# Kernel optimization log

Hardware: AMD Instinct MI355X
Metric: run time of the kernel (lower is better)

## Reference

```python
import jax, jax.numpy as jnp
import numpy as np

NUM_HEADS = 12
HEAD_SIZE = 64
N_EMBED = 768
SEQ_LEN = 2048
BATCH = 4


def setup_inputs() -> dict:
    key = jax.random.key(0)
    ks = jax.random.split(key, 7)
    s = 0.02
    x = jax.random.normal(ks[0], (BATCH, SEQ_LEN, N_EMBED), dtype=jnp.float32)
    # per-head bias-free q/k/v projections: [H, E, D]
    Wq = jax.random.normal(ks[1], (NUM_HEADS, N_EMBED, HEAD_SIZE), dtype=jnp.float32) * s
    Wk = jax.random.normal(ks[2], (NUM_HEADS, N_EMBED, HEAD_SIZE), dtype=jnp.float32) * s
    Wv = jax.random.normal(ks[3], (NUM_HEADS, N_EMBED, HEAD_SIZE), dtype=jnp.float32) * s
    # output projection: Linear(num_heads*head_size, n_embed)
    Wp = jax.random.normal(ks[4], (NUM_HEADS * HEAD_SIZE, N_EMBED), dtype=jnp.float32) * s
    bp = jax.random.normal(ks[5], (N_EMBED,), dtype=jnp.float32) * s
    return {"x": x, "Wq": Wq, "Wk": Wk, "Wv": Wv, "Wp": Wp, "bp": bp}


def reference(x, Wq, Wk, Wv, Wp, bp):
    B, S, E = x.shape
    scale = HEAD_SIZE ** -0.5
    # project all heads at once: [B,H,S,D]
    q = jnp.einsum("bse,hed->bhsd", x, Wq)
    k = jnp.einsum("bse,hed->bhsd", x, Wk)
    v = jnp.einsum("bse,hed->bhsd", x, Wv)
    # scaled dot-product scores [B,H,S,S] with causal mask
    scores = jnp.einsum("bhsd,bhtd->bhst", q, k) * scale
    causal = jnp.tril(jnp.ones((S, S), dtype=bool))
    scores = jnp.where(causal[None, None, :, :], scores, jnp.finfo(scores.dtype).min)
    attn = jax.nn.softmax(scores, axis=-1)
    out = jnp.einsum("bhst,bhtd->bhsd", attn, v)
    # concat heads along feature dim: [B,S,H*D]
    out = out.transpose(0, 2, 1, 3).reshape(B, S, NUM_HEADS * HEAD_SIZE)
    # final projection (dropout rate = 0.0)
    return out @ Wp + bp
```

## Files before the change

kernel.cpp:

```cpp
#include <hip/hip_runtime.h>
#include <hip/hip_bf16.h>


typedef __attribute__((ext_vector_type(8))) short bf16x8;
typedef __attribute__((ext_vector_type(4))) float f32x4;
typedef __attribute__((ext_vector_type(16))) float f32x16;
typedef __attribute__((ext_vector_type(4))) uint u32x4;

#define OFF_XB   0
#define OFF_WT   6291456
#define OFF_WPT  8060928
#define OFF_QKV  8650752
#define OFF_AO   27525120

#define SCALE_LOG2E 0.1803368801111204f

__device__ inline ushort f2bf(float f) {
  __hip_bfloat16 h = __float2bfloat16(f);
  return *reinterpret_cast<ushort*>(&h);
}
__device__ inline uint cvt_pk(float lo, float hi) {
  uint r;
  asm("v_cvt_pk_bf16_f32 %0, %1, %2" : "=v"(r) : "v"(lo), "v"(hi));
  return r;
}
#define GLOAD16(g, l)                                                              \
  __builtin_amdgcn_global_load_lds(                                                \
      (const __attribute__((address_space(1))) uint*)(g),                          \
      (__attribute__((address_space(3))) uint*)(l), 16, 0, 0)

#define WAITBAR(n) asm volatile("s_waitcnt vmcnt(" #n ")\ns_barrier" ::: "memory")
#define ENDBAR()   asm volatile("s_waitcnt lgkmcnt(0)\ns_barrier" ::: "memory")

__global__ __launch_bounds__(256) void cvt_bf16(const float* __restrict__ src,
                                                ushort* __restrict__ dst, int n8) {
  int i = blockIdx.x * 256 + threadIdx.x;
  if (i >= n8) return;
  float4 a = *(const float4*)&src[(size_t)i * 8];
  float4 b = *(const float4*)&src[(size_t)i * 8 + 4];
  u32x4 pk = {cvt_pk(a.x, a.y), cvt_pk(a.z, a.w), cvt_pk(b.x, b.y), cvt_pk(b.z, b.w)};
  *(bf16x8*)&dst[(size_t)i * 8] = __builtin_bit_cast(bf16x8, pk);
}

__global__ __launch_bounds__(256) void transpose_wqkv(const float* __restrict__ Wq,
                                                      const float* __restrict__ Wk,
                                                      const float* __restrict__ Wv,
                                                      ushort* __restrict__ dst) {
  __shared__ ushort tile[64][130];
  int mat = blockIdx.y;
  int te = blockIdx.x;
  const float* src = (mat < 12) ? Wq : (mat < 24) ? Wk : Wv;
  int m12 = mat % 12;
  size_t base = (size_t)m12 * 768 * 64;
  int t = threadIdx.x;
#pragma unroll
  for (int i = 0; i < 16; i++) {
    int idx = i * 256 + t;
    int r = idx >> 6, c = idx & 63;
    tile[r][c] = f2bf(src[base + (size_t)(te * 64 + r) * 64 + c]);
  }
  __syncthreads();
  size_t obase = (size_t)mat * 49152;
#pragma unroll
  for (int i = 0; i < 16; i++) {
    int idx = i * 256 + t;
    int c = idx >> 6, r = idx & 63;
    dst[obase + (size_t)c * 768 + te * 64 + r] = tile[r][c];
  }
}

__global__ __launch_bounds__(256) void transpose_w(const float* __restrict__ src,
                                                   ushort* __restrict__ dst,
                                                   int Edim, int Ddim) {
  __shared__ ushort tile[64][130];
  int ntd = Ddim >> 6;
  int te = blockIdx.x / ntd, td = blockIdx.x % ntd;
  int t = threadIdx.x;
#pragma unroll
  for (int i = 0; i < 16; i++) {
    int idx = i * 256 + t;
    int r = idx >> 6, c = idx & 63;
    tile[r][c] = f2bf(src[(size_t)(te * 64 + r) * Ddim + td * 64 + c]);
  }
  __syncthreads();
#pragma unroll
  for (int i = 0; i < 16; i++) {
    int idx = i * 256 + t;
    int c = idx >> 6, r = idx & 63;
    dst[(size_t)(td * 64 + c) * Edim + te * 64 + r] = tile[r][c];
  }
}

__device__ inline uint swz(uint row) { return (row + (row >> 2)) & 3; }

__global__ __launch_bounds__(128, 2) void gemm_qkv(const ushort* __restrict__ X,
                                                   const ushort* __restrict__ Wt,
                                                   ushort* __restrict__ qkv,
                                                   uint* __restrict__ vtg) {
  __shared__ ushort Ash[2][128 * 32];
  __shared__ ushort Bsh[2][128 * 32];
  int mb = blockIdx.x, nb = blockIdx.y;
  int t = threadIdx.x, w = t >> 6, lane = t & 63, lo = lane & 15, g = lane >> 4;
  const ushort* Ab = X + (size_t)mb * 128 * 768;
  const ushort* Bb = Wt + (size_t)nb * 128 * 768;
  f32x4 acc[4][8];
#pragma unroll
  for (int fi = 0; fi < 4; fi++)
#pragma unroll
    for (int fj = 0; fj < 8; fj++) acc[fi][fj] = (f32x4){0.f, 0.f, 0.f, 0.f};
  uint srow[4], ssc[4];
#pragma unroll
  for (int j = 0; j < 4; j++) {
    uint ci = j * 128 + t;
    srow[j] = ci >> 2;
    ssc[j] = ((ci & 3) ^ swz(ci >> 2)) << 4;
  }

#define QKV_STAGE(tile, bsel)                                                         \
  {                                                                                   \
    int e0 = (tile) * 32;                                                             \
    _Pragma("unroll")                                                                 \
    for (int j = 0; j < 4; j++) {                                                     \
      GLOAD16((const char*)(Ab + (size_t)srow[j] * 768 + e0) + ssc[j],                \
              &Ash[bsel][(j * 128 + w * 64) * 8]);                                    \
      GLOAD16((const char*)(Bb + (size_t)srow[j] * 768 + e0) + ssc[j],                \
              &Bsh[bsel][(j * 128 + w * 64) * 8]);                                    \
    }                                                                                 \
  }

  QKV_STAGE(0, 0);
  QKV_STAGE(1, 1);
  uint rsw = swz(lo) << 4;
  for (int it = 0; it < 24; ++it) {
    if (it < 23) { WAITBAR(8); } else { WAITBAR(0); }
    const ushort* Acur = Ash[it & 1];
    const ushort* Bcur = Bsh[it & 1];
    bf16x8 af[4], bf[8];
#pragma unroll
    for (int fi = 0; fi < 4; fi++) {
      int arow = w * 64 + fi * 16 + lo;
      af[fi] = *(const bf16x8*)((const char*)Acur + arow * 64 + ((g << 4) ^ rsw));
    }
#pragma unroll
    for (int fj = 0; fj < 8; fj++) {
      int brow = fj * 16 + lo;
      bf[fj] = *(const bf16x8*)((const char*)Bcur + brow * 64 + ((g << 4) ^ rsw));
    }
#pragma unroll
    for (int fi = 0; fi < 4; fi++)
#pragma unroll
      for (int fj = 0; fj < 8; fj++)
        acc[fi][fj] = __builtin_amdgcn_mfma_f32_16x16x32_bf16(af[fi], bf[fj], acc[fi][fj], 0, 0, 0);
    if (it < 22) {
      ENDBAR();
      QKV_STAGE(it + 2, it & 1);
    }
  }
#undef QKV_STAGE
#pragma unroll
  for (int fj = 0; fj < 8; fj++) {
    int mat = nb * 2 + (fj >> 2);
    int ty = mat / 12, h = mat % 12;
    int d = (fj & 3) * 16 + lo;
    if (ty < 2) {
#pragma unroll
      for (int fi = 0; fi < 4; fi++)
#pragma unroll
        for (int rr = 0; rr < 4; rr++) {
          int m = mb * 128 + w * 64 + fi * 16 + g * 4 + rr;
          int b = m >> 11, s = m & 2047;
          qkv[(size_t)ty * 6291456 + (size_t)(b * 12 + h) * 131072 + (size_t)s * 64 + d] =
              f2bf(acc[fi][fj][rr]);
        }
    } else {
#pragma unroll
      for (int fi = 0; fi < 4; fi++)
#pragma unroll
        for (int rr = 0; rr < 4; rr += 2) {
          int m = mb * 128 + w * 64 + fi * 16 + g * 4 + rr;
          int b = m >> 11, s = m & 2047;
          uint pk = cvt_pk(acc[fi][fj][rr], acc[fi][fj][rr + 1]);
          vtg[(size_t)(b * 12 + h) * 65536 + (s >> 6) * 2048 + d * 32 + ((s & 63) >> 1)] = pk;
        }
    }
  }
}

__global__ __launch_bounds__(256, 3) void attn_fwd(const ushort* __restrict__ Qg,
                                                   const ushort* __restrict__ Kg,
                                                   const uint* __restrict__ Vtg,
                                                   ushort* __restrict__ ao) {
  __shared__ ushort Ksh[2][64 * 72];
  __shared__ uint Vsh[2][64 * 36];
  int x = blockIdx.x;
  int head = x % 48;
  int qb = 15 - x / 48;
  int T = 2 * qb + 2;
  int t = threadIdx.x, w = t >> 6, q31 = t & 31, hi = (t & 63) >> 5;
  const ushort* Q = Qg + (size_t)head * 131072;
  const ushort* K = Kg + (size_t)head * 131072;
  const uint* V = Vtg + (size_t)head * 65536;
  int qstart = qb * 128 + 32 * w;
  int qg = qstart + q31;
  bf16x8 qf[4];
#pragma unroll
  for (int s = 0; s < 4; s++)
    qf[s] = *(const bf16x8*)&Q[(size_t)qg * 64 + s * 16 + hi * 8];
  bf16x8 ones;
#pragma unroll
  for (int i = 0; i < 8; i++) ones[i] = (short)0x3F80;
  f32x16 oacc[2], lacc;
#pragma unroll
  for (int r = 0; r < 16; r++) { oacc[0][r] = 0.f; oacc[1][r] = 0.f; lacc[r] = 0.f; }
  int sr = t >> 3, sc = t & 7;
  bf16x8 kreg[2];
  u32x4 vreg[2];
#pragma unroll
  for (int i = 0; i < 2; i++) {
    kreg[i] = *(const bf16x8*)&K[(size_t)(i * 32 + sr) * 64 + sc * 8];
    vreg[i] = *(const u32x4*)&V[(i * 32 + sr) * 32 + sc * 4];
  }
#pragma unroll
  for (int i = 0; i < 2; i++) {
    *(bf16x8*)&Ksh[0][(i * 32 + sr) * 72 + sc * 8] = kreg[i];
    *(u32x4*)&Vsh[0][(i * 32 + sr) * 36 + sc * 4] = vreg[i];
  }
  for (int kb = 0; kb < T; kb++) {
    __syncthreads();
    if (kb + 1 < T) {
      int t1 = (kb + 1) * 64;
#pragma unroll
      for (int i = 0; i < 2; i++) {
        kreg[i] = *(const bf16x8*)&K[(size_t)(t1 + i * 32 + sr) * 64 + sc * 8];
        vreg[i] = *(const u32x4*)&V[(kb + 1) * 2048 + (i * 32 + sr) * 32 + sc * 4];
      }
    }
    int t0 = kb * 64;
    if (t0 <= qstart + 31) {
      const ushort* Kb = Ksh[kb & 1];
      const uint* Vb = Vsh[kb & 1];
      bool act1 = (t0 + 32 <= qstart + 31);
      f32x16 st0, st1;
#pragma unroll
      for (int r = 0; r < 16; r++) { st0[r] = 0.f; st1[r] = 0.f; }
#pragma unroll
      for (int s = 0; s < 4; s++) {
        bf16x8 kf = *(const bf16x8*)&Kb[q31 * 72 + s * 16 + hi * 8];
        st0 = __builtin_amdgcn_mfma_f32_32x32x16_bf16(kf, qf[s], st0, 0, 0, 0);
      }
      if (act1) {
#pragma unroll
        for (int s = 0; s < 4; s++) {
          bf16x8 kf = *(const bf16x8*)&Kb[(32 + q31) * 72 + s * 16 + hi * 8];
          st1 = __builtin_amdgcn_mfma_f32_32x32x16_bf16(kf, qf[s], st1, 0, 0, 0);
        }
      }
      if (t0 + 31 > qstart) {
        int base = t0 - qstart;
#pragma unroll
        for (int r = 0; r < 16; r++) {
          int crow = (r & 3) + 8 * (r >> 2) + 4 * hi;
          if (base + crow > q31) st0[r] = -3e38f;
        }
      }
      if (act1 && (t0 + 63 > qstart)) {
        int base = t0 + 32 - qstart;
#pragma unroll
        for (int r = 0; r < 16; r++) {
          int crow = (r & 3) + 8 * (r >> 2) + 4 * hi;
          if (base + crow > q31) st1[r] = -3e38f;
        }
      }
#pragma unroll
      for (int r = 0; r < 16; r++)
        st0[r] = __builtin_amdgcn_exp2f(st0[r] * SCALE_LOG2E);
      if (act1) {
#pragma unroll
        for (int r = 0; r < 16; r++)
          st1[r] = __builtin_amdgcn_exp2f(st1[r] * SCALE_LOG2E);
      }
      int ns = act1 ? 4 : 2;
      bf16x8 paf[4];
#pragma unroll
      for (int s = 0; s < 4; s++) {
        if (s < ns) {
          const f32x16& sv = (s < 2) ? st0 : st1;
          int rb = (s & 1) * 8;
          uint a = cvt_pk(sv[rb + 0], sv[rb + 1]);
          uint b2 = cvt_pk(sv[rb + 2], sv[rb + 3]);
          uint c = cvt_pk(sv[rb + 4], sv[rb + 5]);
          uint d = cvt_pk(sv[rb + 6], sv[rb + 7]);
          asm volatile("v_permlane32_swap_b32 %0, %1" : "+v"(a), "+v"(c));
          asm volatile("v_permlane32_swap_b32 %0, %1" : "+v"(b2), "+v"(d));
          u32x4 u4 = {a, b2, c, d};
          paf[s] = __builtin_bit_cast(bf16x8, u4);
        }
      }
#pragma unroll
      for (int s = 0; s < 4; s++) {
        if (s < ns) {
          lacc = __builtin_amdgcn_mfma_f32_32x32x16_bf16(paf[s], ones, lacc, 0, 0, 0);
#pragma unroll
          for (int dt = 0; dt < 2; dt++) {
            bf16x8 vf = *(const bf16x8*)&Vb[(dt * 32 + q31) * 36 + s * 8 + hi * 4];
            oacc[dt] = __builtin_amdgcn_mfma_f32_32x32x16_bf16(paf[s], vf, oacc[dt], 0, 0, 0);
          }
        }
      }
    }
    if (kb + 1 < T) {
      int b2 = (kb + 1) & 1;
#pragma unroll
      for (int i = 0; i < 2; i++) {
        *(bf16x8*)&Ksh[b2][(i * 32 + sr) * 72 + sc * 8] = kreg[i];
        *(u32x4*)&Vsh[b2][(i * 32 + sr) * 36 + sc * 4] = vreg[i];
      }
    }
  }
  int hh = head % 12, bb = head / 12;
#pragma unroll
  for (int dt = 0; dt < 2; dt++)
#pragma unroll
    for (int r = 0; r < 16; r++) {
      int qr = qstart + (r & 3) + 8 * (r >> 2) + 4 * hi;
      ao[(size_t)(bb * 2048 + qr) * 768 + hh * 64 + dt * 32 + q31] =
          f2bf(oacc[dt][r] / lacc[r]);
    }
}

__global__ __launch_bounds__(128, 2) void gemm_out(const ushort* __restrict__ A,
                                                   const ushort* __restrict__ Bt,
                                                   const float* __restrict__ bias,
                                                   float* __restrict__ out) {
  __shared__ ushort Ash[2][128 * 32];
  __shared__ ushort Bsh[2][128 * 32];
  int mb = blockIdx.x, nb = blockIdx.y;
  int t = threadIdx.x, w = t >> 6, lane = t & 63, lo = lane & 15, g = lane >> 4;
  const ushort* Ab = A + (size_t)mb * 128 * 768;
  const ushort* Bb = Bt + (size_t)nb * 128 * 768;
  f32x4 acc[4][8];
#pragma unroll
  for (int fi = 0; fi < 4; fi++)
#pragma unroll
    for (int fj = 0; fj < 8; fj++) acc[fi][fj] = (f32x4){0.f, 0.f, 0.f, 0.f};
  uint srow[4], ssc[4];
#pragma unroll
  for (int j = 0; j < 4; j++) {
    uint ci = j * 128 + t;
    srow[j] = ci >> 2;
    ssc[j] = ((ci & 3) ^ swz(ci >> 2)) << 4;
  }

#define OUT_STAGE(tile, bsel)                                                         \
  {                                                                                   \
    int e0 = (tile) * 32;                                                             \
    _Pragma("unroll")                                                                 \
    for (int j = 0; j < 4; j++) {                                                     \
      GLOAD16((const char*)(Ab + (size_t)srow[j] * 768 + e0) + ssc[j],                \
              &Ash[bsel][(j * 128 + w * 64) * 8]);                                    \
      GLOAD16((const char*)(Bb + (size_t)srow[j] * 768 + e0) + ssc[j],                \
              &Bsh[bsel][(j * 128 + w * 64) * 8]);                                    \
    }                                                                                 \
  }

  OUT_STAGE(0, 0);
  OUT_STAGE(1, 1);
  uint rsw = swz(lo) << 4;
  for (int it = 0; it < 24; ++it) {
    if (it < 23) { WAITBAR(8); } else { WAITBAR(0); }
    const ushort* Acur = Ash[it & 1];
    const ushort* Bcur = Bsh[it & 1];
    bf16x8 af[4], bf[8];
#pragma unroll
    for (int fi = 0; fi < 4; fi++) {
      int arow = w * 64 + fi * 16 + lo;
      af[fi] = *(const bf16x8*)((const char*)Acur + arow * 64 + ((g << 4) ^ rsw));
    }
#pragma unroll
    for (int fj = 0; fj < 8; fj++) {
      int brow = fj * 16 + lo;
      bf[fj] = *(const bf16x8*)((const char*)Bcur + brow * 64 + ((g << 4) ^ rsw));
    }
#pragma unroll
    for (int fi = 0; fi < 4; fi++)
#pragma unroll
      for (int fj = 0; fj < 8; fj++)
        acc[fi][fj] = __builtin_amdgcn_mfma_f32_16x16x32_bf16(af[fi], bf[fj], acc[fi][fj], 0, 0, 0);
    if (it < 22) {
      ENDBAR();
      OUT_STAGE(it + 2, it & 1);
    }
  }
#undef OUT_STAGE
#pragma unroll
  for (int fj = 0; fj < 8; fj++) {
    int col = nb * 128 + fj * 16 + lo;
    float bv = bias[col];
#pragma unroll
    for (int fi = 0; fi < 4; fi++)
#pragma unroll
      for (int rr = 0; rr < 4; rr++) {
        int m = mb * 128 + w * 64 + fi * 16 + g * 4 + rr;
        out[(size_t)m * 768 + col] = acc[fi][fj][rr] + bv;
      }
  }
}

extern "C" void kernel_launch(void* const* d_in, const int* in_sizes, int n_in,
                              void* d_out, int out_size, void* d_ws, size_t ws_size,
                              hipStream_t stream) {
  const float* x  = (const float*)d_in[0];
  const float* Wq = (const float*)d_in[1];
  const float* Wk = (const float*)d_in[2];
  const float* Wv = (const float*)d_in[3];
  const float* Wp = (const float*)d_in[4];
  const float* bp = (const float*)d_in[5];
  float* out = (float*)d_out;
  ushort* ws = (ushort*)d_ws;

  ushort* xb  = ws + OFF_XB;
  ushort* wt  = ws + OFF_WT;
  ushort* wpt = ws + OFF_WPT;
  ushort* qkv = ws + OFF_QKV;
  uint*   vt  = (uint*)(ws + OFF_QKV + 2 * 6291456);
  ushort* ao  = ws + OFF_AO;

  cvt_bf16<<<dim3(3072), 256, 0, stream>>>(x, xb, 786432);
  transpose_wqkv<<<dim3(12, 36), 256, 0, stream>>>(Wq, Wk, Wv, wt);
  transpose_w<<<dim3(144), 256, 0, stream>>>(Wp, wpt, 768, 768);

  gemm_qkv<<<dim3(64, 18), 128, 0, stream>>>(xb, wt, qkv, vt);
  attn_fwd<<<dim3(768), 256, 0, stream>>>(qkv, qkv + 6291456, vt, ao);
  gemm_out<<<dim3(64, 6), 128, 0, stream>>>(ao, wpt, bp, out);
}
```

Measured before the change: 129.4 us.

## Give each wave private LDS tiles in projection GEMMs to drop barriers

After: 143.5 us. +10.9%, slower.

```diff
diff --git a/kernel.cpp b/kernel.cpp
--- a/kernel.cpp
+++ b/kernel.cpp
@@ -29,8 +29,8 @@
       (const __attribute__((address_space(1))) uint*)(g),                          \
       (__attribute__((address_space(3))) uint*)(l), 16, 0, 0)
 
-#define WAITBAR(n) asm volatile("s_waitcnt vmcnt(" #n ")\ns_barrier" ::: "memory")
-#define ENDBAR()   asm volatile("s_waitcnt lgkmcnt(0)\ns_barrier" ::: "memory")
+#define WAITN(n)  asm volatile("s_waitcnt vmcnt(" #n ")" ::: "memory")
+#define LGKM0()   asm volatile("s_waitcnt lgkmcnt(0)" ::: "memory")
 
 __global__ __launch_bounds__(256) void cvt_bf16(const float* __restrict__ src,
                                                 ushort* __restrict__ dst, int n8) {
@@ -93,58 +93,63 @@
 
 __device__ inline uint swz(uint row) { return (row + (row >> 2)) & 3; }
 
-__global__ __launch_bounds__(128, 2) void gemm_qkv(const ushort* __restrict__ X,
-                                                   const ushort* __restrict__ Wt,
-                                                   ushort* __restrict__ qkv,
-                                                   uint* __restrict__ vtg) {
-  __shared__ ushort Ash[2][128 * 32];
-  __shared__ ushort Bsh[2][128 * 32];
+__global__ __launch_bounds__(128) void gemm_qkv(const ushort* __restrict__ X,
+                                                const ushort* __restrict__ Wt,
+                                                ushort* __restrict__ qkv,
+                                                uint* __restrict__ vtg) {
+  __shared__ ushort Aw[2][2][64 * 32];
+  __shared__ ushort Bw[2][2][128 * 32];
   int mb = blockIdx.x, nb = blockIdx.y;
   int t = threadIdx.x, w = t >> 6, lane = t & 63, lo = lane & 15, g = lane >> 4;
-  const ushort* Ab = X + (size_t)mb * 128 * 768;
-  const ushort* Bb = Wt + (size_t)nb * 128 * 768;
+  const char* Ab = (const char*)(X + ((size_t)mb * 128 + w * 64) * 768);
+  const char* Bb = (const char*)(Wt + (size_t)nb * 128 * 768);
   f32x4 acc[4][8];
 #pragma unroll
   for (int fi = 0; fi < 4; fi++)
 #pragma unroll
     for (int fj = 0; fj < 8; fj++) acc[fi][fj] = (f32x4){0.f, 0.f, 0.f, 0.f};
-  uint srow[4], ssc[4];
+  uint aoff[4], boff[8];
 #pragma unroll
   for (int j = 0; j < 4; j++) {
-    uint ci = j * 128 + t;
-    srow[j] = ci >> 2;
-    ssc[j] = ((ci & 3) ^ swz(ci >> 2)) << 4;
-  }
-
-#define QKV_STAGE(tile, bsel)                                                         \
-  {                                                                                   \
-    int e0 = (tile) * 32;                                                             \
-    _Pragma("unroll")                                                                 \
-    for (int j = 0; j < 4; j++) {                                                     \
-      GLOAD16((const char*)(Ab + (size_t)srow[j] * 768 + e0) + ssc[j],                \
-              &Ash[bsel][(j * 128 + w * 64) * 8]);                                    \
-      GLOAD16((const char*)(Bb + (size_t)srow[j] * 768 + e0) + ssc[j],                \
-              &Bsh[bsel][(j * 128 + w * 64) * 8]);                                    \
-    }                                                                                 \
+    uint ci = j * 64 + lane, row = ci >> 2, c = ci & 3;
+    aoff[j] = row * 1536 + (((c ^ swz(row))) << 4);
+  }
+#pragma unroll
+  for (int j = 0; j < 8; j++) {
+    uint ci = j * 64 + lane, row = ci >> 2, c = ci & 3;
+    boff[j] = row * 1536 + (((c ^ swz(row))) << 4);
+  }
+  ushort* Awb = &Aw[w][0][0];
+  ushort* Bwb = &Bw[w][0][0];
+
+#define QKV_STAGE(tile, buf)                                                        \
+  {                                                                                 \
+    uint e2 = (uint)(tile) * 64;                        \
+    _Pragma("unroll")                                                               \
+    for (int j = 0; j < 4; j++)                                                     \
+      GLOAD16(Ab + aoff[j] + e2, Awb + (buf) * 2048 + j * 512);                     \
+    _Pragma("unroll")                                                               \
+    for (int j = 0; j < 8; j++)                                                     \
+      GLOAD16(Bb + boff[j] + e2, Bwb + (buf) * 4096 + j * 512);                     \
   }
 
   QKV_STAGE(0, 0);
   QKV_STAGE(1, 1);
   uint rsw = swz(lo) << 4;
   for (int it = 0; it < 24; ++it) {
-    if (it < 23) { WAITBAR(8); } else { WAITBAR(0); }
-    const ushort* Acur = Ash[it & 1];
-    const ushort* Bcur = Bsh[it & 1];
+    if (it < 23) { WAITN(12); } else { WAITN(0); }
+    const char* Acur = (const char*)(Awb + (it & 1) * 2048);
+    const char* Bcur = (const char*)(Bwb + (it & 1) * 4096);
     bf16x8 af[4], bf[8];
 #pragma unroll
     for (int fi = 0; fi < 4; fi++) {
-      int arow = w * 64 + fi * 16 + lo;
-      af[fi] = *(const bf16x8*)((const char*)Acur + arow * 64 + ((g << 4) ^ rsw));
+      uint arow = fi * 16 + lo;
+      af[fi] = *(const bf16x8*)(Acur + arow * 64 + ((g << 4) ^ rsw));
     }
 #pragma unroll
     for (int fj = 0; fj < 8; fj++) {
-      int brow = fj * 16 + lo;
-      bf[fj] = *(const bf16x8*)((const char*)Bcur + brow * 64 + ((g << 4) ^ rsw));
+      uint brow = fj * 16 + lo;
+      bf[fj] = *(const bf16x8*)(Bcur + brow * 64 + ((g << 4) ^ rsw));
     }
 #pragma unroll
     for (int fi = 0; fi < 4; fi++)
@@ -152,7 +157,7 @@
       for (int fj = 0; fj < 8; fj++)
         acc[fi][fj] = __builtin_amdgcn_mfma_f32_16x16x32_bf16(af[fi], bf[fj], acc[fi][fj], 0, 0, 0);
     if (it < 22) {
-      ENDBAR();
+      LGKM0();
       QKV_STAGE(it + 2, it & 1);
     }
   }
@@ -328,58 +333,63 @@
     }
 }
 
-__global__ __launch_bounds__(128, 2) void gemm_out(const ushort* __restrict__ A,
-                                                   const ushort* __restrict__ Bt,
-                                                   const float* __restrict__ bias,
-                                                   float* __restrict__ out) {
-  __shared__ ushort Ash[2][128 * 32];
-  __shared__ ushort Bsh[2][128 * 32];
+__global__ __launch_bounds__(128) void gemm_out(const ushort* __restrict__ A,
+                                                const ushort* __restrict__ Bt,
+                                                const float* __restrict__ bias,
+                                                float* __restrict__ out) {
+  __shared__ ushort Aw[2][2][64 * 32];
+  __shared__ ushort Bw[2][2][128 * 32];
   int mb = blockIdx.x, nb = blockIdx.y;
   int t = threadIdx.x, w = t >> 6, lane = t & 63, lo = lane & 15, g = lane >> 4;
-  const ushort* Ab = A + (size_t)mb * 128 * 768;
-  const ushort* Bb = Bt + (size_t)nb * 128 * 768;
+  const char* Ab = (const char*)(A + ((size_t)mb * 128 + w * 64) * 768);
+  const char* Bb = (const char*)(Bt + (size_t)nb * 128 * 768);
   f32x4 acc[4][8];
 #pragma unroll
   for (int fi = 0; fi < 4; fi++)
 #pragma unroll
     for (int fj = 0; fj < 8; fj++) acc[fi][fj] = (f32x4){0.f, 0.f, 0.f, 0.f};
-  uint srow[4], ssc[4];
+  uint aoff[4], boff[8];
 #pragma unroll
   for (int j = 0; j < 4; j++) {
-    uint ci = j * 128 + t;
-    srow[j] = ci >> 2;
-    ssc[j] = ((ci & 3) ^ swz(ci >> 2)) << 4;
-  }
-
-#define OUT_STAGE(tile, bsel)                                                         \
-  {                                                                                   \
-    int e0 = (tile) * 32;                                                             \
-    _Pragma("unroll")                                                                 \
-    for (int j = 0; j < 4; j++) {                                                     \
-      GLOAD16((const char*)(Ab + (size_t)srow[j] * 768 + e0) + ssc[j],                \
-              &Ash[bsel][(j * 128 + w * 64) * 8]);                                    \
-      GLOAD16((const char*)(Bb + (size_t)srow[j] * 768 + e0) + ssc[j],                \
-              &Bsh[bsel][(j * 128 + w * 64) * 8]);                                    \
-    }                                                                                 \
+    uint ci = j * 64 + lane, row = ci >> 2, c = ci & 3;
+    aoff[j] = row * 1536 + (((c ^ swz(row))) << 4);
+  }
+#pragma unroll
+  for (int j = 0; j < 8; j++) {
+    uint ci = j * 64 + lane, row = ci >> 2, c = ci & 3;
+    boff[j] = row * 1536 + (((c ^ swz(row))) << 4);
+  }
+  ushort* Awb = &Aw[w][0][0];
+  ushort* Bwb = &Bw[w][0][0];
+
+#define OUT_STAGE(tile, buf)                                                        \
+  {                                                                                 \
+    uint e2 = (uint)(tile) * 64;                                                    \
+    _Pragma("unroll")                                                               \
+    for (int j = 0; j < 4; j++)                                                     \
+      GLOAD16(Ab + aoff[j] + e2, Awb + (buf) * 2048 + j * 512);                     \
+    _Pragma("unroll")                                                               \
+    for (int j = 0; j < 8; j++)                                                     \
+      GLOAD16(Bb + boff[j] + e2, Bwb + (buf) * 4096 + j * 512);                     \
   }
 
   OUT_STAGE(0, 0);
   OUT_STAGE(1, 1);
   uint rsw = swz(lo) << 4;
   for (int it = 0; it < 24; ++it) {
-    if (it < 23) { WAITBAR(8); } else { WAITBAR(0); }
-    const ushort* Acur = Ash[it & 1];
-    const ushort* Bcur = Bsh[it & 1];
+    if (it < 23) { WAITN(12); } else { WAITN(0); }
+    const char* Acur = (const char*)(Awb + (it & 1) * 2048);
+    const char* Bcur = (const char*)(Bwb + (it & 1) * 4096);
     bf16x8 af[4], bf[8];
 #pragma unroll
     for (int fi = 0; fi < 4; fi++) {
-      int arow = w * 64 + fi * 16 + lo;
-      af[fi] = *(const bf16x8*)((const char*)Acur + arow * 64 + ((g << 4) ^ rsw));
+      uint arow = fi * 16 + lo;
+      af[fi] = *(const bf16x8*)(Acur + arow * 64 + ((g << 4) ^ rsw));
     }
 #pragma unroll
     for (int fj = 0; fj < 8; fj++) {
-      int brow = fj * 16 + lo;
-      bf[fj] = *(const bf16x8*)((const char*)Bcur + brow * 64 + ((g << 4) ^ rsw));
+      uint brow = fj * 16 + lo;
+      bf[fj] = *(const bf16x8*)(Bcur + brow * 64 + ((g << 4) ^ rsw));
     }
 #pragma unroll
     for (int fi = 0; fi < 4; fi++)
@@ -387,7 +397,7 @@
       for (int fj = 0; fj < 8; fj++)
         acc[fi][fj] = __builtin_amdgcn_mfma_f32_16x16x32_bf16(af[fi], bf[fj], acc[fi][fj], 0, 0, 0);
     if (it < 22) {
-      ENDBAR();
+      LGKM0();
       OUT_STAGE(it + 2, it & 1);
     }
   }
```

## Restructure QKV GEMM into 512-thread 128x256 tiles with interleaved load/MFMA phases

Applied to the files above, without the earlier changes.

Measured after the change: 137.5 us. +6.2%, slower.

```diff
diff --git a/kernel.cpp b/kernel.cpp
--- a/kernel.cpp
+++ b/kernel.cpp
@@ -24,13 +24,16 @@
   asm("v_cvt_pk_bf16_f32 %0, %1, %2" : "=v"(r) : "v"(lo), "v"(hi));
   return r;
 }
-#define GLOAD16(g, l)                                                              \
+#define GLOAD16(gp, lp)                                                            \
   __builtin_amdgcn_global_load_lds(                                                \
-      (const __attribute__((address_space(1))) uint*)(g),                          \
-      (__attribute__((address_space(3))) uint*)(l), 16, 0, 0)
+      (const __attribute__((address_space(1))) uint*)(gp),                         \
+      (__attribute__((address_space(3))) uint*)(lp), 16, 0, 0)
 
 #define WAITBAR(n) asm volatile("s_waitcnt vmcnt(" #n ")\ns_barrier" ::: "memory")
 #define ENDBAR()   asm volatile("s_waitcnt lgkmcnt(0)\ns_barrier" ::: "memory")
+#define LGKM0()    asm volatile("s_waitcnt lgkmcnt(0)" ::: "memory")
+#define BAR()      __builtin_amdgcn_s_barrier()
+#define SCHED0()   __builtin_amdgcn_sched_barrier(0)
 
 __global__ __launch_bounds__(256) void cvt_bf16(const float* __restrict__ src,
                                                 ushort* __restrict__ dst, int n8) {
@@ -92,82 +95,155 @@
 }
 
 __device__ inline uint swz(uint row) { return (row + (row >> 2)) & 3; }
-
-__global__ __launch_bounds__(128, 2) void gemm_qkv(const ushort* __restrict__ X,
+__device__ inline uint swz3(uint r) { return (r + (r >> 3)) & 7; }
+
+__global__ __launch_bounds__(512, 2) void gemm_qkv(const ushort* __restrict__ X,
                                                    const ushort* __restrict__ Wt,
                                                    ushort* __restrict__ qkv,
                                                    uint* __restrict__ vtg) {
-  __shared__ ushort Ash[2][128 * 32];
-  __shared__ ushort Bsh[2][128 * 32];
-  int mb = blockIdx.x, nb = blockIdx.y;
+  __shared__ ushort Ash[2][2][4096];
+  __shared__ ushort Bsh[2][2][8192];
+  int bx = blockIdx.x;
+  int wg = (bx & 7) * 72 + (bx >> 3);
+  int nb = wg / 64, mb = wg % 64;
   int t = threadIdx.x, w = t >> 6, lane = t & 63, lo = lane & 15, g = lane >> 4;
-  const ushort* Ab = X + (size_t)mb * 128 * 768;
-  const ushort* Bb = Wt + (size_t)nb * 128 * 768;
-  f32x4 acc[4][8];
+  int wm = w >> 2, wn = w & 3;
+  const char* Ab = (const char*)X + (size_t)mb * 128 * 1536;
+  const char* Bb = (const char*)Wt + (size_t)nb * 256 * 1536;
+  f32x4 acc[4][4];
 #pragma unroll
   for (int fi = 0; fi < 4; fi++)
 #pragma unroll
-    for (int fj = 0; fj < 8; fj++) acc[fi][fj] = (f32x4){0.f, 0.f, 0.f, 0.f};
-  uint srow[4], ssc[4];
-#pragma unroll
-  for (int j = 0; j < 4; j++) {
-    uint ci = j * 128 + t;
-    srow[j] = ci >> 2;
-    ssc[j] = ((ci & 3) ^ swz(ci >> 2)) << 4;
-  }
-
-#define QKV_STAGE(tile, bsel)                                                         \
-  {                                                                                   \
-    int e0 = (tile) * 32;                                                             \
-    _Pragma("unroll")                                                                 \
-    for (int j = 0; j < 4; j++) {                                                     \
-      GLOAD16((const char*)(Ab + (size_t)srow[j] * 768 + e0) + ssc[j],                \
-              &Ash[bsel][(j * 128 + w * 64) * 8]);                                    \
-      GLOAD16((const char*)(Bb + (size_t)srow[j] * 768 + e0) + ssc[j],                \
-              &Bsh[bsel][(j * 128 + w * 64) * 8]);                                    \
-    }                                                                                 \
-  }
-
-  QKV_STAGE(0, 0);
-  QKV_STAGE(1, 1);
-  uint rsw = swz(lo) << 4;
-  for (int it = 0; it < 24; ++it) {
-    if (it < 23) { WAITBAR(8); } else { WAITBAR(0); }
-    const ushort* Acur = Ash[it & 1];
-    const ushort* Bcur = Bsh[it & 1];
-    bf16x8 af[4], bf[8];
-#pragma unroll
-    for (int fi = 0; fi < 4; fi++) {
-      int arow = w * 64 + fi * 16 + lo;
-      af[fi] = *(const bf16x8*)((const char*)Acur + arow * 64 + ((g << 4) ^ rsw));
-    }
-#pragma unroll
-    for (int fj = 0; fj < 8; fj++) {
-      int brow = fj * 16 + lo;
-      bf[fj] = *(const bf16x8*)((const char*)Bcur + brow * 64 + ((g << 4) ^ rsw));
-    }
-#pragma unroll
-    for (int fi = 0; fi < 4; fi++)
-#pragma unroll
-      for (int fj = 0; fj < 8; fj++)
-        acc[fi][fj] = __builtin_amdgcn_mfma_f32_16x16x32_bf16(af[fi], bf[fj], acc[fi][fj], 0, 0, 0);
-    if (it < 22) {
-      ENDBAR();
-      QKV_STAGE(it + 2, it & 1);
-    }
-  }
-#undef QKV_STAGE
-#pragma unroll
-  for (int fj = 0; fj < 8; fj++) {
-    int mat = nb * 2 + (fj >> 2);
-    int ty = mat / 12, h = mat % 12;
-    int d = (fj & 3) * 16 + lo;
+    for (int fj = 0; fj < 4; fj++) acc[fi][fj] = (f32x4){0.f, 0.f, 0.f, 0.f};
+  uint arw = (uint)t >> 3, acx = ((uint)t & 7) ^ swz3((uint)t >> 3);
+  uint aoff = ((arw & 31) + ((arw >> 5) << 6)) * 1536 + acx * 16;
+  uint brw0 = (uint)t >> 3, brw1 = ((uint)t + 512) >> 3;
+  uint boff0 = brw0 * 1536 + ((((uint)t & 7) ^ swz3(brw0)) << 4);
+  uint boff1 = brw1 * 1536 + ((((uint)t & 7) ^ swz3(brw1)) << 4);
+  uint aro[4], asw[4], bro[4], bsw[4];
+#pragma unroll
+  for (int fi = 0; fi < 4; fi++) {
+    uint r = wm * 64 + fi * 16 + lo;
+    uint h = (r >> 5) & 1;
+    uint rw = (r & 31) | ((r >> 6) << 5);
+    aro[fi] = h * 8192 + rw * 128;
+    asw[fi] = swz3(rw);
+  }
+#pragma unroll
+  for (int fj = 0; fj < 4; fj++) {
+    uint cc = wn * 64 + fj * 16 + lo;
+    uint h = cc >> 7, rw = cc & 127;
+    bro[fj] = h * 16384 + rw * 128;
+    bsw[fj] = swz3(rw);
+  }
+
+#define STAGE_A(kt, h)                                                              \
+  GLOAD16(Ab + aoff + (h) * 49152 + (kt) * 128,                                     \
+          (char*)Ash + ((kt) & 1) * 16384 + (h) * 8192 + t * 16)
+#define STAGE_B(kt, h)                                                              \
+  {                                                                                 \
+    GLOAD16(Bb + boff0 + (h) * 196608 + (kt) * 128,                                 \
+            (char*)Bsh + ((kt) & 1) * 32768 + (h) * 16384 + t * 16);                \
+    GLOAD16(Bb + boff1 + (h) * 196608 + (kt) * 128,                                 \
+            (char*)Bsh + ((kt) & 1) * 32768 + (h) * 16384 + 8192 + t * 16);         \
+  }
+#define AREAD(fi, s, db)                                                            \
+  (*(const bf16x8*)((const char*)Ash + (db) * 16384 + aro[fi] +                     \
+                    ((((s) * 4 + g) ^ asw[fi]) << 4)))
+#define BREAD(fj, s, db)                                                            \
+  (*(const bf16x8*)((const char*)Bsh + (db) * 32768 + bro[fj] +                     \
+                    ((((s) * 4 + g) ^ bsw[fj]) << 4)))
+#define MFMA8(fi)                                                                   \
+  {                                                                                 \
+    __builtin_amdgcn_s_setprio(1);                                                  \
+    _Pragma("unroll")                                                               \
+    for (int fj = 0; fj < 4; fj++) {                                                \
+      acc[fi][fj] = __builtin_amdgcn_mfma_f32_16x16x32_bf16(af0, bfr[fj][0],        \
+                                                            acc[fi][fj], 0, 0, 0);  \
+      acc[fi][fj] = __builtin_amdgcn_mfma_f32_16x16x32_bf16(af1, bfr[fj][1],        \
+                                                            acc[fi][fj], 0, 0, 0);  \
+    }                                                                               \
+    __builtin_amdgcn_s_setprio(0);                                                  \
+  }
+#define PHASE_MID() { BAR(); LGKM0(); SCHED0(); }
+
+  STAGE_A(0, 0); STAGE_B(0, 0); STAGE_B(0, 1); STAGE_A(0, 1);
+  STAGE_A(1, 0); STAGE_B(1, 0); STAGE_B(1, 1);
+  WAITBAR(6);
+
+  bf16x8 bfr[4][2];
+  bf16x8 af0, af1;
+  for (int it = 0; it < 5; ++it) {
+    int E = 2 * it, O = 2 * it + 1;
+    af0 = AREAD(0, 0, 0); af1 = AREAD(0, 1, 0);
+#pragma unroll
+    for (int fj = 0; fj < 4; fj++) { bfr[fj][0] = BREAD(fj, 0, 0); bfr[fj][1] = BREAD(fj, 1, 0); }
+    STAGE_A(O, 1);
+    PHASE_MID(); MFMA8(0); BAR();
+    af0 = AREAD(1, 0, 0); af1 = AREAD(1, 1, 0);
+    STAGE_B(E + 2, 0);
+    PHASE_MID(); MFMA8(1); WAITBAR(8);
+    af0 = AREAD(2, 0, 0); af1 = AREAD(2, 1, 0);
+    STAGE_B(E + 2, 1);
+    PHASE_MID(); MFMA8(2); BAR();
+    af0 = AREAD(3, 0, 0); af1 = AREAD(3, 1, 0);
+    STAGE_A(E + 2, 0);
+    PHASE_MID(); MFMA8(3); WAITBAR(6);
+    af0 = AREAD(0, 0, 1); af1 = AREAD(0, 1, 1);
+#pragma unroll
+    for (int fj = 0; fj < 4; fj++) { bfr[fj][0] = BREAD(fj, 0, 1); bfr[fj][1] = BREAD(fj, 1, 1); }
+    STAGE_A(E + 2, 1);
+    PHASE_MID(); MFMA8(0); BAR();
+    af0 = AREAD(1, 0, 1); af1 = AREAD(1, 1, 1);
+    STAGE_B(O + 2, 0);
+    PHASE_MID(); MFMA8(1); WAITBAR(8);
+    af0 = AREAD(2, 0, 1); af1 = AREAD(2, 1, 1);
+    STAGE_B(O + 2, 1);
+    PHASE_MID(); MFMA8(2); BAR();
+    af0 = AREAD(3, 0, 1); af1 = AREAD(3, 1, 1);
+    STAGE_A(O + 2, 0);
+    PHASE_MID(); MFMA8(3); WAITBAR(6);
+  }
+  {
+    af0 = AREAD(0, 0, 0); af1 = AREAD(0, 1, 0);
+#pragma unroll
+    for (int fj = 0; fj < 4; fj++) { bfr[fj][0] = BREAD(fj, 0, 0); bfr[fj][1] = BREAD(fj, 1, 0); }
+    STAGE_A(11, 1);
+    PHASE_MID(); MFMA8(0); BAR();
+    af0 = AREAD(1, 0, 0); af1 = AREAD(1, 1, 0);
+    PHASE_MID(); MFMA8(1); WAITBAR(6);
+    af0 = AREAD(2, 0, 0); af1 = AREAD(2, 1, 0);
+    PHASE_MID(); MFMA8(2); BAR();
+    af0 = AREAD(3, 0, 0); af1 = AREAD(3, 1, 0);
+    PHASE_MID(); MFMA8(3); WAITBAR(1);
+    af0 = AREAD(0, 0, 1); af1 = AREAD(0, 1, 1);
+#pragma unroll
+    for (int fj = 0; fj < 4; fj++) { bfr[fj][0] = BREAD(fj, 0, 1); bfr[fj][1] = BREAD(fj, 1, 1); }
+    PHASE_MID(); MFMA8(0); BAR();
+    af0 = AREAD(1, 0, 1); af1 = AREAD(1, 1, 1);
+    PHASE_MID(); MFMA8(1); WAITBAR(0);
+    af0 = AREAD(2, 0, 1); af1 = AREAD(2, 1, 1);
+    PHASE_MID(); MFMA8(2); BAR();
+    af0 = AREAD(3, 0, 1); af1 = AREAD(3, 1, 1);
+    PHASE_MID(); MFMA8(3);
+  }
+#undef STAGE_A
+#undef STAGE_B
+#undef AREAD
+#undef BREAD
+#undef MFMA8
+#undef PHASE_MID
+  int mat = nb * 4 + wn;
+  int ty = mat / 12, h = mat % 12;
+#pragma unroll
+  for (int fj = 0; fj < 4; fj++) {
+    int d = fj * 16 + lo;
     if (ty < 2) {
 #pragma unroll
       for (int fi = 0; fi < 4; fi++)
 #pragma unroll
         for (int rr = 0; rr < 4; rr++) {
-          int m = mb * 128 + w * 64 + fi * 16 + g * 4 + rr;
+          int m = mb * 128 + wm * 64 + fi * 16 + g * 4 + rr;
           int b = m >> 11, s = m & 2047;
           qkv[(size_t)ty * 6291456 + (size_t)(b * 12 + h) * 131072 + (size_t)s * 64 + d] =
               f2bf(acc[fi][fj][rr]);
@@ -177,7 +253,7 @@
       for (int fi = 0; fi < 4; fi++)
 #pragma unroll
         for (int rr = 0; rr < 4; rr += 2) {
-          int m = mb * 128 + w * 64 + fi * 16 + g * 4 + rr;
+          int m = mb * 128 + wm * 64 + fi * 16 + g * 4 + rr;
           int b = m >> 11, s = m & 2047;
           uint pk = cvt_pk(acc[fi][fj][rr], acc[fi][fj][rr + 1]);
           vtg[(size_t)(b * 12 + h) * 65536 + (s >> 6) * 2048 + d * 32 + ((s & 63) >> 1)] = pk;
@@ -429,7 +505,7 @@
   transpose_wqkv<<<dim3(12, 36), 256, 0, stream>>>(Wq, Wk, Wv, wt);
   transpose_w<<<dim3(144), 256, 0, stream>>>(Wp, wpt, 768, 768);
 
-  gemm_qkv<<<dim3(64, 18), 128, 0, stream>>>(xb, wt, qkv, vt);
+  gemm_qkv<<<dim3(576), 512, 0, stream>>>(xb, wt, qkv, vt);
   attn_fwd<<<dim3(768), 256, 0, stream>>>(qkv, qkv + 6291456, vt, ao);
   gemm_out<<<dim3(64, 6), 128, 0, stream>>>(ao, wpt, bp, out);
 }
```

## Read K/V tiles directly from global memory, dropping LDS staging and block syncs

Applied to the files above, without the earlier changes.

Measured after the change: 202.0 us. +56.1%, slower.

```diff
diff --git a/kernel.cpp b/kernel.cpp
--- a/kernel.cpp
+++ b/kernel.cpp
@@ -190,18 +190,16 @@
                                                    const ushort* __restrict__ Kg,
                                                    const uint* __restrict__ Vtg,
                                                    ushort* __restrict__ ao) {
-  __shared__ ushort Ksh[2][64 * 72];
-  __shared__ uint Vsh[2][64 * 36];
   int x = blockIdx.x;
   int head = x % 48;
   int qb = 15 - x / 48;
-  int T = 2 * qb + 2;
   int t = threadIdx.x, w = t >> 6, q31 = t & 31, hi = (t & 63) >> 5;
   const ushort* Q = Qg + (size_t)head * 131072;
   const ushort* K = Kg + (size_t)head * 131072;
   const uint* V = Vtg + (size_t)head * 65536;
   int qstart = qb * 128 + 32 * w;
   int qg = qstart + q31;
+  int Tw = ((qstart + 31) >> 6) + 1;
   bf16x8 qf[4];
 #pragma unroll
   for (int s = 0; s < 4; s++)
@@ -212,108 +210,75 @@
   f32x16 oacc[2], lacc;
 #pragma unroll
   for (int r = 0; r < 16; r++) { oacc[0][r] = 0.f; oacc[1][r] = 0.f; lacc[r] = 0.f; }
-  int sr = t >> 3, sc = t & 7;
-  bf16x8 kreg[2];
-  u32x4 vreg[2];
-#pragma unroll
-  for (int i = 0; i < 2; i++) {
-    kreg[i] = *(const bf16x8*)&K[(size_t)(i * 32 + sr) * 64 + sc * 8];
-    vreg[i] = *(const u32x4*)&V[(i * 32 + sr) * 32 + sc * 4];
-  }
-#pragma unroll
-  for (int i = 0; i < 2; i++) {
-    *(bf16x8*)&Ksh[0][(i * 32 + sr) * 72 + sc * 8] = kreg[i];
-    *(u32x4*)&Vsh[0][(i * 32 + sr) * 36 + sc * 4] = vreg[i];
-  }
-  for (int kb = 0; kb < T; kb++) {
-    __syncthreads();
-    if (kb + 1 < T) {
-      int t1 = (kb + 1) * 64;
-#pragma unroll
-      for (int i = 0; i < 2; i++) {
-        kreg[i] = *(const bf16x8*)&K[(size_t)(t1 + i * 32 + sr) * 64 + sc * 8];
-        vreg[i] = *(const u32x4*)&V[(kb + 1) * 2048 + (i * 32 + sr) * 32 + sc * 4];
-      }
-    }
+  for (int kb = 0; kb < Tw; kb++) {
     int t0 = kb * 64;
-    if (t0 <= qstart + 31) {
-      const ushort* Kb = Ksh[kb & 1];
-      const uint* Vb = Vsh[kb & 1];
-      bool act1 = (t0 + 32 <= qstart + 31);
-      f32x16 st0, st1;
-#pragma unroll
-      for (int r = 0; r < 16; r++) { st0[r] = 0.f; st1[r] = 0.f; }
+    bool act1 = (t0 + 32 <= qstart + 31);
+    const ushort* Kt = K + (size_t)t0 * 64;
+    const uint* Vt = V + kb * 2048;
+    f32x16 st0, st1;
+#pragma unroll
+    for (int r = 0; r < 16; r++) { st0[r] = 0.f; st1[r] = 0.f; }
+#pragma unroll
+    for (int s = 0; s < 4; s++) {
+      bf16x8 kf = *(const bf16x8*)&Kt[(size_t)q31 * 64 + s * 16 + hi * 8];
+      st0 = __builtin_amdgcn_mfma_f32_32x32x16_bf16(kf, qf[s], st0, 0, 0, 0);
+    }
+    if (act1) {
 #pragma unroll
       for (int s = 0; s < 4; s++) {
-        bf16x8 kf = *(const bf16x8*)&Kb[q31 * 72 + s * 16 + hi * 8];
-        st0 = __builtin_amdgcn_mfma_f32_32x32x16_bf16(kf, qf[s], st0, 0, 0, 0);
-      }
-      if (act1) {
-#pragma unroll
-        for (int s = 0; s < 4; s++) {
-          bf16x8 kf = *(const bf16x8*)&Kb[(32 + q31) * 72 + s * 16 + hi * 8];
-          st1 = __builtin_amdgcn_mfma_f32_32x32x16_bf16(kf, qf[s], st1, 0, 0, 0);
-        }
-      }
-      if (t0 + 31 > qstart) {
-        int base = t0 - qstart;
-#pragma unroll
-        for (int r = 0; r < 16; r++) {
-          int crow = (r & 3) + 8 * (r >> 2) + 4 * hi;
-          if (base + crow > q31) st0[r] = -3e38f;
-        }
-      }
-      if (act1 && (t0 + 63 > qstart)) {
-        int base = t0 + 32 - qstart;
-#pragma unroll
-        for (int r = 0; r < 16; r++) {
-          int crow = (r & 3) + 8 * (r >> 2) + 4 * hi;
-          if (base + crow > q31) st1[r] = -3e38f;
-        }
-      }
+        bf16x8 kf = *(const bf16x8*)&Kt[(size_t)(32 + q31) * 64 + s * 16 + hi * 8];
+        st1 = __builtin_amdgcn_mfma_f32_32x32x16_bf16(kf, qf[s], st1, 0, 0, 0);
+      }
+    }
+    if (t0 + 31 > qstart) {
+      int base = t0 - qstart;
+#pragma unroll
+      for (int r = 0; r < 16; r++) {
+        int crow = (r & 3) + 8 * (r >> 2) + 4 * hi;
+        if (base + crow > q31) st0[r] = -3e38f;
+      }
+    }
+    if (act1 && (t0 + 63 > qstart)) {
+      int base = t0 + 32 - qstart;
+#pragma unroll
+      for (int r = 0; r < 16; r++) {
+        int crow = (r & 3) + 8 * (r >> 2) + 4 * hi;
+        if (base + crow > q31) st1[r] = -3e38f;
+      }
+    }
+#pragma unroll
+    for (int r = 0; r < 16; r++)
+      st0[r] = __builtin_amdgcn_exp2f(st0[r] * SCALE_LOG2E);
+    if (act1) {
 #pragma unroll
       for (int r = 0; r < 16; r++)
-        st0[r] = __builtin_amdgcn_exp2f(st0[r] * SCALE_LOG2E);
-      if (act1) {
-#pragma unroll
-        for (int r = 0; r < 16; r++)
-          st1[r] = __builtin_amdgcn_exp2f(st1[r] * SCALE_LOG2E);
-      }
-      int ns = act1 ? 4 : 2;
-      bf16x8 paf[4];
-#pragma unroll
-      for (int s = 0; s < 4; s++) {
-        if (s < ns) {
-          const f32x16& sv = (s < 2) ? st0 : st1;
-          int rb = (s & 1) * 8;
-          uint a = cvt_pk(sv[rb + 0], sv[rb + 1]);
-          uint b2 = cvt_pk(sv[rb + 2], sv[rb + 3]);
-          uint c = cvt_pk(sv[rb + 4], sv[rb + 5]);
-          uint d = cvt_pk(sv[rb + 6], sv[rb + 7]);
-          asm volatile("v_permlane32_swap_b32 %0, %1" : "+v"(a), "+v"(c));
-          asm volatile("v_permlane32_swap_b32 %0, %1" : "+v"(b2), "+v"(d));
-          u32x4 u4 = {a, b2, c, d};
-          paf[s] = __builtin_bit_cast(bf16x8, u4);
-        }
-      }
-#pragma unroll
-      for (int s = 0; s < 4; s++) {
-        if (s < ns) {
-          lacc = __builtin_amdgcn_mfma_f32_32x32x16_bf16(paf[s], ones, lacc, 0, 0, 0);
-#pragma unroll
-          for (int dt = 0; dt < 2; dt++) {
-            bf16x8 vf = *(const bf16x8*)&Vb[(dt * 32 + q31) * 36 + s * 8 + hi * 4];
-            oacc[dt] = __builtin_amdgcn_mfma_f32_32x32x16_bf16(paf[s], vf, oacc[dt], 0, 0, 0);
-          }
-        }
-      }
-    }
-    if (kb + 1 < T) {
-      int b2 = (kb + 1) & 1;
-#pragma unroll
-      for (int i = 0; i < 2; i++) {
-        *(bf16x8*)&Ksh[b2][(i * 32 + sr) * 72 + sc * 8] = kreg[i];
-        *(u32x4*)&Vsh[b2][(i * 32 + sr) * 36 + sc * 4] = vreg[i];
+        st1[r] = __builtin_amdgcn_exp2f(st1[r] * SCALE_LOG2E);
+    }
+    int ns = act1 ? 4 : 2;
+    bf16x8 paf[4];
+#pragma unroll
+    for (int s = 0; s < 4; s++) {
+      if (s < ns) {
+        const f32x16& sv = (s < 2) ? st0 : st1;
+        int rb = (s & 1) * 8;
+        uint a = cvt_pk(sv[rb + 0], sv[rb + 1]);
+        uint b2 = cvt_pk(sv[rb + 2], sv[rb + 3]);
+        uint c = cvt_pk(sv[rb + 4], sv[rb + 5]);
+        uint d = cvt_pk(sv[rb + 6], sv[rb + 7]);
+        asm volatile("v_permlane32_swap_b32 %0, %1" : "+v"(a), "+v"(c));
+        asm volatile("v_permlane32_swap_b32 %0, %1" : "+v"(b2), "+v"(d));
+        u32x4 u4 = {a, b2, c, d};
+        paf[s] = __builtin_bit_cast(bf16x8, u4);
+      }
+    }
+#pragma unroll
+    for (int s = 0; s < 4; s++) {
+      if (s < ns) {
+        lacc = __builtin_amdgcn_mfma_f32_32x32x16_bf16(paf[s], ones, lacc, 0, 0, 0);
+        bf16x8 vf0 = *(const bf16x8*)&Vt[(size_t)q31 * 32 + s * 8 + hi * 4];
+        oacc[0] = __builtin_amdgcn_mfma_f32_32x32x16_bf16(paf[s], vf0, oacc[0], 0, 0, 0);
+        bf16x8 vf1 = *(const bf16x8*)&Vt[(size_t)(32 + q31) * 32 + s * 8 + hi * 4];
+        oacc[1] = __builtin_amdgcn_mfma_f32_32x32x16_bf16(paf[s], vf1, oacc[1], 0, 0, 0);
       }
     }
   }
```
